# Optimization experiments

Hardware: AMD Instinct MI355X
Metric: run time of the kernel (lower is better)

Reference implementation:

```python
import jax, jax.numpy as jnp
import numpy as np

B, L, D = 512, 200, 128
N_ITEMS = 50001
T_STEPS = 4
TAU = 2.0
STEP = 1
V_TH = 1.0
SG_ALPHA = 4.0  # spikingjelly default surrogate.Sigmoid alpha


@jax.custom_vjp
def spike(x):
    return (x >= 0.0).astype(x.dtype)

def _spike_fwd(x):
    return spike(x), x

def _spike_bwd(x, g):
    s = jax.nn.sigmoid(SG_ALPHA * x)
    return (g * SG_ALPHA * s * (1.0 - s),)

spike.defvjp(_spike_fwd, _spike_bwd)


def lif_multistep(x):
    """Multi-step LIF (hard reset to 0, detach_reset). x: [T, ...] -> spikes [T, ...]."""
    def step(v, xt):
        v = v + (xt - v) / TAU  # charge (v_reset = 0)
        s = spike(v - V_TH)
        v = v - jax.lax.stop_gradient(s) * v  # hard reset, detached spike
        return v, s
    v0 = jnp.zeros_like(x[0])
    _, spikes = jax.lax.scan(step, v0, x)
    return spikes


def layernorm(x, g, b, eps=1e-5):
    m = x.mean(-1, keepdims=True)
    v = x.var(-1, keepdims=True)
    return (x - m) / jnp.sqrt(v + eps) * g + b


def _build_session_graphs(rng):
    lens = rng.integers(50, L + 1, size=B)
    item_seq = np.zeros((B, L), dtype=np.int64)
    for b in range(B):
        item_seq[b, :lens[b]] = rng.integers(1, N_ITEMS, size=lens[b])
    alias = np.zeros((B, L), dtype=np.int64)
    items = np.zeros((B, L), dtype=np.int64)
    A = np.zeros((B, L, 2 * L), dtype=np.float32)
    for b in range(B):
        u = item_seq[b]
        node = np.unique(u)  # sorted
        items[b, :len(node)] = node
        alias[b] = np.searchsorted(node, u)
        uA = np.zeros((L, L), dtype=np.float32)
        for i in range(L - 1):
            if u[i + 1] == 0:
                break
            r = np.searchsorted(node, u[i])
            c = np.searchsorted(node, u[i + 1])
            uA[r, c] = 1.0
        sin = uA.sum(0); sin[sin == 0] = 1.0
        sout = uA.sum(1); sout[sout == 0] = 1.0
        A[b, :, :L] = (uA / sin).T          # u_A_in.T
        A[b, :, L:] = ((uA.T / sout)).T     # u_A_out.T
    mask = item_seq > 0
    return A, alias, items, mask, lens.astype(np.int64)


def setup_inputs() -> dict:
    rng = np.random.default_rng(0)
    A, alias, items, mask, lens = _build_session_graphs(rng)
    stdv = 1.0 / np.sqrt(D)
    key = jax.random.key(0)
    ks = jax.random.split(key, 24)
    u = lambda k, shape: jax.random.uniform(k, shape, jnp.float32, -stdv, stdv)
    item_emb = u(ks[0], (N_ITEMS, D)).at[0].set(0.0)  # padding_idx=0
    return {
        "A": jnp.asarray(A),
        "alias_inputs": jnp.asarray(alias),
        "items": jnp.asarray(items),
        "mask": jnp.asarray(mask),
        "item_seq_len": jnp.asarray(lens),
        "item_emb": item_emb,
        "W_in": u(ks[1], (D, D)), "b_in": u(ks[2], (D,)),
        "W_out": u(ks[3], (D, D)), "b_out": u(ks[4], (D,)),
        "w_ih": u(ks[5], (3 * D, 2 * D)), "w_hh": u(ks[6], (3 * D, D)),
        "b_ih": u(ks[7], (3 * D,)), "b_hh": u(ks[8], (3 * D,)),
        "b_iah": u(ks[9], (D,)), "b_ioh": u(ks[10], (D,)),
        "W1": u(ks[11], (D, D)), "W2": u(ks[12], (D, D)),
        "W3": u(ks[13], (1, D)), "Wt": u(ks[14], (D, 2 * D)),
        "g_q": u(ks[15], (D,)), "beta_q": u(ks[16], (D,)),
        "g_sh": u(ks[17], (2 * D,)), "beta_sh": u(ks[18], (2 * D,)),
    }


def _forward(A, alias_inputs, items, mask, item_seq_len, item_emb,
             W_in, b_in, W_out, b_out, w_ih, w_hh, b_ih, b_hh, b_iah, b_ioh,
             W1, W2, W3, Wt, g_q, beta_q, g_sh, beta_sh):
    hidden = item_emb[items]  # [B,L,D]
    for _ in range(STEP):
        ein = hidden @ W_in.T + b_in
        eout = hidden @ W_out.T + b_out
        input_in = jnp.einsum('bij,bjd->bid', A[:, :, :L], ein) + b_iah
        input_out = jnp.einsum('bij,bjd->bid', A[:, :, L:], eout) + b_ioh
        inputs = jnp.concatenate([input_in, input_out], axis=-1)  # [B,L,2D]
        gi = inputs @ w_ih.T + b_ih  # [B,L,3D]
        gh = hidden @ w_hh.T + b_hh
        i_r, i_i, i_n = jnp.split(gi, 3, axis=-1)
        h_r, h_i, h_n = jnp.split(gh, 3, axis=-1)
        r = jax.nn.sigmoid(i_r + h_r)
        z = jax.nn.sigmoid(i_i + h_i)
        n = jnp.tanh(i_n + r * h_n)
        hidden = (1.0 - z) * hidden + z * n
    seq_hidden = jnp.take_along_axis(hidden, alias_inputs[..., None], axis=1)  # [B,L,D]
    ht = jnp.take_along_axis(seq_hidden, (item_seq_len - 1)[:, None, None], axis=1)[:, 0]  # [B,D]
    Qb = (ht @ W1.T)[:, None, :] + seq_hidden @ W2.T  # [B,L,D]
    Q = jnp.broadcast_to(Qb[None], (T_STEPS, B, L, D))
    Qs = lif_multistep(layernorm(Q, g_q, beta_q))
    alpha = Qs @ W3.T  # [T,B,L,1]
    mf = mask.astype(alpha.dtype)
    a = jnp.sum(alpha * seq_hidden[None] * mf[None, :, :, None], axis=2)  # [T,B,D]
    ht_T = jnp.broadcast_to(ht[None], (T_STEPS, B, D))
    sh = jnp.concatenate([a, ht_T], axis=-1)  # [T,B,2D]
    sh = layernorm(lif_multistep(sh), g_sh, beta_sh)
    return (sh @ Wt.T).mean(0)  # [B,D]


def reference(A, alias_inputs, items, mask, item_seq_len, item_emb,
              W_in, b_in, W_out, b_out, w_ih, w_hh, b_ih, b_hh, b_iah, b_ioh,
              W1, W2, W3, Wt, g_q, beta_q, g_sh, beta_sh):
    return _forward(A, alias_inputs, items, mask, item_seq_len, item_emb,
                    W_in, b_in, W_out, b_out, w_ih, w_hh, b_ih, b_hh, b_iah, b_ioh,
                    W1, W2, W3, Wt, g_q, beta_q, g_sh, beta_sh)
```

## Files before the change

### kernel.cpp

```cpp
#include <hip/hip_runtime.h>
#include <hip/hip_bf16.h>
#include <cstdint>
#include <cstddef>

#define B_ 512
#define L_ 200
#define D_ 128
#define M_ (B_*L_)
#define T_ 4

typedef short bf16x8 __attribute__((ext_vector_type(8)));
typedef unsigned short u16x8 __attribute__((ext_vector_type(8)));
typedef float f32x4 __attribute__((ext_vector_type(4)));

__device__ __forceinline__ float bf2f(unsigned short u){
  union { unsigned int i; float f; } c; c.i = ((unsigned int)u)<<16; return c.f;
}
__device__ __forceinline__ unsigned short f2bf(float f){
  union { float f; unsigned int i; } c; c.f = f;
  unsigned int r = c.i + 0x7FFFu + ((c.i>>16)&1u);
  return (unsigned short)(r>>16);
}
__device__ __forceinline__ float wsum(float v){
  #pragma unroll
  for (int m=1;m<64;m<<=1) v += __shfl_xor(v, m, 64);
  return v;
}
__device__ __forceinline__ void gload_lds16(const void* g, void* l){
  __builtin_amdgcn_global_load_lds(
      (const __attribute__((address_space(1))) void*)g,
      (__attribute__((address_space(3))) void*)l, 16, 0, 0);
}

__global__ __launch_bounds__(256)
void gemm_bt(const unsigned short* __restrict__ A, int lda,
             const unsigned short* __restrict__ Bt, int ldb,
             const float* __restrict__ bias,
             unsigned short* __restrict__ C, int ldc, int K,
             const int* __restrict__ mlimit, const int* __restrict__ gidx)
{
  const int m0 = blockIdx.y * 128;
  const int Mv = mlimit ? *mlimit : (1<<30);
  if (m0 >= Mv) return;
  __shared__ __align__(16) short sAs[2][128*32];
  __shared__ __align__(16) short sBs[2][128*32];
  const int tid = threadIdx.x;
  const int n0 = blockIdx.x * 128;
  const int lane = tid & 63;
  const int w = tid >> 6;
  const int wr = (w>>1)*64, wc = (w&1)*64;

  f32x4 acc[4][4];
  #pragma unroll
  for (int i=0;i<4;i++)
    #pragma unroll
    for (int j=0;j<4;j++) acc[i][j] = (f32x4){0.f,0.f,0.f,0.f};

  const int c1 = tid, c2 = tid + 256;
  const int r1 = c1>>2, s1 = c1&3, k1 = ((s1 ^ ((r1>>1)&3))&3)<<3;
  const int r2 = c2>>2, s2 = c2&3, k2 = ((s2 ^ ((r2>>1)&3))&3)<<3;
  int ar1 = m0 + r1, ar2 = m0 + r2;
  if (gidx){ ar1 = (ar1 < Mv) ? gidx[ar1] : 0; ar2 = (ar2 < Mv) ? gidx[ar2] : 0; }
  const int fr = lane & 15;
  const int fq = lane >> 4;
  const int fk = ((fq ^ ((fr>>1)&3))&3)<<3;

  auto stage = [&](int t){
    const int buf = t & 1, ks = t << 5;
    gload_lds16(A  + (size_t)ar1*lda + ks + k1, sAs[buf] + (size_t)c1*8);
    gload_lds16(A  + (size_t)ar2*lda + ks + k2, sAs[buf] + (size_t)c2*8);
    gload_lds16(Bt + (size_t)(n0 + r1)*ldb + ks + k1, sBs[buf] + (size_t)c1*8);
    gload_lds16(Bt + (size_t)(n0 + r2)*ldb + ks + k2, sBs[buf] + (size_t)c2*8);
  };
  const int nT = K >> 5;
  stage(0);
  __syncthreads();
  for (int t=0; t<nT; ++t){
    if (t+1 < nT) stage(t+1);
    const short* a_ = sAs[t&1];
    const short* b_ = sBs[t&1];
    bf16x8 af[4], bfr[4];
    #pragma unroll
    for (int i=0;i<4;i++){
      af[i]  = *(const bf16x8*)(a_ + (wr + i*16 + fr)*32 + fk);
      bfr[i] = *(const bf16x8*)(b_ + (wc + i*16 + fr)*32 + fk);
    }
    #pragma unroll
    for (int i=0;i<4;i++)
      #pragma unroll
      for (int j=0;j<4;j++)
        acc[i][j] = __builtin_amdgcn_mfma_f32_16x16x32_bf16(af[i], bfr[j], acc[i][j], 0,0,0);
    __syncthreads();
  }

  const int orow = fq<<2;
  #pragma unroll
  for (int i=0;i<4;i++){
    #pragma unroll
    for (int j=0;j<4;j++){
      const int gn = n0 + wc + j*16 + fr;
      const float bv = bias ? bias[gn] : 0.f;
      #pragma unroll
      for (int v=0;v<4;v++){
        const int gm = m0 + wr + i*16 + orow + v;
        C[(size_t)gm*ldc + gn] = f2bf(acc[i][j][v] + bv);
      }
    }
  }
}

__global__ __launch_bounds__(128)
void k_prepW(const float* __restrict__ w_ih, const float* __restrict__ w_hh,
             const float* __restrict__ W_in, const float* __restrict__ W_out,
             const float* __restrict__ b_in, const float* __restrict__ b_out,
             const float* __restrict__ b_ih, const float* __restrict__ b_hh,
             const float* __restrict__ b_iah, const float* __restrict__ b_ioh,
             const float* __restrict__ W2,
             const int* __restrict__ alias, const int* __restrict__ lens,
             unsigned short* __restrict__ Wbig, float* __restrict__ biasBase,
             float* __restrict__ uIn, float* __restrict__ uOut,
             unsigned short* __restrict__ w2b, int* __restrict__ nb)
{
  const int p = blockIdx.x, t = threadIdx.x;
  if (p < 128) w2b[p*128 + t] = f2bf(W2[p*128 + t]);
  const int dim = p>>2, g = p&3;
  const int row = (g==0) ? dim : (g==1) ? 128+dim : 256+dim;
  const bool has_ih = (g!=3), has_hh = (g!=2);
  __shared__ float wl[128], wrg[128], red[3][128];
  wl[t]  = has_ih ? w_ih[(size_t)row*256 + t]       : 0.f;
  wrg[t] = has_ih ? w_ih[(size_t)row*256 + 128 + t] : 0.f;
  __syncthreads();
  float cin = 0.f, cout = 0.f;
  if (has_ih) {
    for (int m=0;m<128;m++){
      cin  += wl[m]  * W_in [m*128 + t];
      cout += wrg[m] * W_out[m*128 + t];
    }
  }
  Wbig[(size_t)p*384 +       t] = f2bf(cin);
  Wbig[(size_t)p*384 + 128 + t] = f2bf(cout);
  Wbig[(size_t)p*384 + 256 + t] = f2bf(has_hh ? w_hh[(size_t)row*128 + t] : 0.f);
  red[0][t] = wl[t]*b_iah[t] + wrg[t]*b_ioh[t];
  red[1][t] = wl[t]*b_in[t];
  red[2][t] = wrg[t]*b_out[t];
  __syncthreads();
  if (t == 0) {
    float v=0.f, ui=0.f, uo=0.f;
    for (int k=0;k<128;k++){ v += red[0][k]; ui += red[1][k]; uo += red[2][k]; }
    float bb;
    if (g==0)      bb = b_ih[dim]     + b_hh[dim]     + v;
    else if (g==1) bb = b_ih[128+dim] + b_hh[128+dim] + v;
    else if (g==2) bb = b_ih[256+dim] + v;
    else           bb = b_hh[256+dim];
    biasBase[p] = bb;
    uIn[p]  = has_ih ? ui : 0.f;
    uOut[p] = has_ih ? uo : 0.f;
  }
  if (t < 64) {
    const int len = lens[p];
    int m = 0;
    for (int l=t; l<len; l+=64) m = max(m, alias[p*L_ + l]);
    #pragma unroll
    for (int o=1;o<64;o<<=1) m = max(m, __shfl_xor(m, o, 64));
    if (t==0) nb[p] = m + 1;
  }
}

__global__ __launch_bounds__(512)
void k_scan(const int* __restrict__ nb, const int* __restrict__ lens,
            int* __restrict__ nbase, int* __restrict__ vbase)
{
  __shared__ int A[2][512], Bv[2][512];
  const int t = threadIdx.x;
  const int a0 = nb[t], b0 = lens[t];
  A[0][t] = a0; Bv[0][t] = b0;
  __syncthreads();
  int cur = 0;
  for (int off=1; off<512; off<<=1){
    const int nxt = cur^1;
    A[nxt][t]  = A[cur][t]  + (t>=off ? A[cur][t-off]  : 0);
    Bv[nxt][t] = Bv[cur][t] + (t>=off ? Bv[cur][t-off] : 0);
    __syncthreads();
    cur = nxt;
  }
  nbase[t] = A[cur][t] - a0;
  vbase[t] = Bv[cur][t] - b0;
  if (t==511){ nbase[512] = A[cur][511]; vbase[512] = Bv[cur][511]; }
}

__global__ __launch_bounds__(1024)
void k_aggemb(const int* __restrict__ alias, const int* __restrict__ items,
              const int* __restrict__ lens, const float* __restrict__ emb,
              const int* __restrict__ nb, const int* __restrict__ nbase,
              const int* __restrict__ vbase,
              unsigned short* __restrict__ X3, unsigned char* __restrict__ cf,
              int* __restrict__ gidx)
{
  const int b = blockIdx.x, tid = threadIdx.x;
  __shared__ unsigned short hl[L_*128];
  __shared__ int al[L_], it[L_];
  __shared__ unsigned bmIn[L_*8], bmOut[L_*8];
  if (tid < L_) { al[tid] = alias[b*L_ + tid]; it[tid] = items[b*L_ + tid]; }
  for (int i=tid; i<L_*8; i+=1024){ bmIn[i]=0u; bmOut[i]=0u; }
  __syncthreads();
  const int len = lens[b], nB = nb[b], base = nbase[b];
  if (tid < len) gidx[vbase[b] + tid] = base + al[tid];
  if (tid < len-1) {
    const int r = al[tid], c = al[tid+1];
    atomicOr(&bmIn[c*8 + (r>>5)],  1u<<(r&31));
    atomicOr(&bmOut[r*8 + (c>>5)], 1u<<(c&31));
  }
  const int rr = tid>>5, cc = (tid&31)<<2;
  for (int s=0; s<nB; s+=32) {
    const int j = s + rr;
    if (j < nB) {
      const float4 v = *(const float4*)(emb + (size_t)it[j]*128 + cc);
      ushort4 o; o.x=f2bf(v.x); o.y=f2bf(v.y); o.z=f2bf(v.z); o.w=f2bf(v.w);
      *(ushort4*)(hl + j*128 + cc) = o;
      *(ushort4*)(X3 + (size_t)(base + j)*384 + 256 + cc) = o;
    }
  }
  __syncthreads();
  const int g = tid >> 7, d = tid & 127;
  for (int s=0; s<nB; s+=8) {
    const int i = s + g;
    if (i < nB) {
      float si=0.f, so=0.f; int ci=0, co=0;
      #pragma unroll
      for (int wd=0; wd<8; ++wd) {
        unsigned word = bmIn[i*8+wd];
        while (word) { int j = __ffs(word)-1; word &= word-1u;
          si += bf2f(hl[(wd*32+j)*128 + d]); ci++; }
        word = bmOut[i*8+wd];
        while (word) { int j = __ffs(word)-1; word &= word-1u;
          so += bf2f(hl[(wd*32+j)*128 + d]); co++; }
      }
      unsigned short* xr = X3 + (size_t)(base + i)*384;
      xr[d]       = f2bf(si / (float)(ci>0?ci:1));
      xr[128 + d] = f2bf(so / (float)(co>0?co:1));
      if (d == 0) cf[base + i] = (unsigned char)((ci>0?1:0) | (co>0?2:0));
    }
  }
}

__global__ __launch_bounds__(512)
void k_gates_gru(const unsigned short* __restrict__ X3,
                 const unsigned short* __restrict__ Wbig,
                 const float* __restrict__ biasBase,
                 const float* __restrict__ uIn,
                 const float* __restrict__ uOut,
                 const unsigned char* __restrict__ cf,
                 unsigned short* __restrict__ hidden,
                 const int* __restrict__ mlimit)
{
  const int m0 = blockIdx.y * 128;
  if (m0 >= *mlimit) return;
  __shared__ __align__(16) short sA[2][128*32];
  __shared__ __align__(16) short sB[2][256*32];
  const int tid = threadIdx.x;
  const int p0 = blockIdx.x * 256;
  const int lane = tid & 63;
  const int w = tid >> 6;
  const int wr  = (w>>2)*64;
  const int wcp = (w&3)*64;
  const int fr = lane & 15;
  const int fq = lane >> 4;
  const int fk = ((fq ^ ((fr>>1)&3))&3)<<3;

  f32x4 acc[4][4];
  #pragma unroll
  for (int i=0;i<4;i++)
    #pragma unroll
    for (int j=0;j<4;j++) acc[i][j] = (f32x4){0.f,0.f,0.f,0.f};

  const int ra = tid>>2, sa_ = tid&3, ka = ((sa_ ^ ((ra>>1)&3))&3)<<3;
  const int c1 = tid + 512, rb1 = c1>>2, sb1 = c1&3, kb1 = ((sb1 ^ ((rb1>>1)&3))&3)<<3;

  auto stage = [&](int t){
    const int buf = t & 1, ks = t << 5;
    gload_lds16(X3   + (size_t)(m0 + ra )*384 + ks + ka , sA[buf] + (size_t)tid*8);
    gload_lds16(Wbig + (size_t)(p0 + ra )*384 + ks + ka , sB[buf] + (size_t)tid*8);
    gload_lds16(Wbig + (size_t)(p0 + rb1)*384 + ks + kb1, sB[buf] + (size_t)(c1-512)*8 + 512*8);
  };
  stage(0);
  __syncthreads();
  for (int t=0; t<12; ++t){
    if (t < 11) stage(t+1);
    const short* a_ = sA[t&1];
    const short* b_ = sB[t&1];
    bf16x8 af[4], bfr[4];
    #pragma unroll
    for (int i=0;i<4;i++){
      af[i]  = *(const bf16x8*)(a_ + (wr  + i*16 + fr)*32 + fk);
      bfr[i] = *(const bf16x8*)(b_ + (wcp + i*16 + fr)*32 + fk);
    }
    #pragma unroll
    for (int i=0;i<4;i++)
      #pragma unroll
      for (int j=0;j<4;j++)
        acc[i][j] = __builtin_amdgcn_mfma_f32_16x16x32_bf16(af[i], bfr[j], acc[i][j], 0,0,0);
    __syncthreads();
  }

  const bool q0b = (lane & 1), q1b = (lane & 2);
  #pragma unroll
  for (int j=0;j<4;j++){
    const int dim = (p0>>2) + (w&3)*16 + j*4 + ((lane>>2)&3);
    const float4 bb = *(const float4*)(biasBase + dim*4);
    const float4 bi = *(const float4*)(uIn  + dim*4);
    const float4 bo = *(const float4*)(uOut + dim*4);
    #pragma unroll
    for (int i=0;i<4;i++){
      const float a0=acc[i][j][0], a1=acc[i][j][1], a2=acc[i][j][2], a3=acc[i][j][3];
      const float t0=__shfl_xor(a0,1), t1=__shfl_xor(a1,1), t2=__shfl_xor(a2,1), t3=__shfl_xor(a3,1);
      const float s0 = q0b? t1:a0, s1 = q0b? a1:t0, s2 = q0b? t3:a2, s3 = q0b? a3:t2;
      const float u0=__shfl_xor(s0,2), u1=__shfl_xor(s1,2), u2=__shfl_xor(s2,2), u3=__shfl_xor(s3,2);
      float G0 = q1b? u2:s0, G1 = q1b? u3:s1, G2 = q1b? s2:u0, G3 = q1b? s3:u1;
      const int row = m0 + wr + i*16 + fq*4 + (lane&3);
      const unsigned c = cf[row];
      const float fi = (c&1) ? 1.f : 0.f, fo = (c&2) ? 1.f : 0.f;
      G0 += bb.x + fi*bi.x + fo*bo.x;
      G1 += bb.y + fi*bi.y + fo*bo.y;
      G2 += bb.z + fi*bi.z + fo*bo.z;
      G3 += bb.w;
      const float h = bf2f(X3[(size_t)row*384 + 256 + dim]);
      const float r = 1.f/(1.f+__expf(-G0));
      const float z = 1.f/(1.f+__expf(-G1));
      const float x = G2 + r*G3;
      const float n = 1.f - 2.f/(__expf(2.f*x)+1.f);
      hidden[(size_t)row*128 + dim] = f2bf((1.f-z)*h + z*n);
    }
  }
}

__global__ __launch_bounds__(1024)
void k_attn(const unsigned short* __restrict__ Q0,
            const unsigned short* __restrict__ hidden, const int* __restrict__ gidx,
            const int* __restrict__ lens, const int* __restrict__ vbase,
            const float* __restrict__ W1,
            const float* __restrict__ g_q, const float* __restrict__ beta_q,
            const float* __restrict__ W3,
            const float* __restrict__ g_sh, const float* __restrict__ beta_sh,
            const float* __restrict__ Wt, float* __restrict__ out)
{
  const int b = blockIdx.x, tid = threadIdx.x;
  const int w = tid>>6, lane = tid&63;
  __shared__ float a_acc[16][T_][128];
  __shared__ float htv[128], htw[128];
  __shared__ float ys[256];
  __shared__ float part[T_][4];
  const int len = lens[b], vb = vbase[b];
  for (int i=tid; i<16*T_*128; i+=1024) ((float*)a_acc)[i] = 0.f;
  if (tid < 128) htv[tid] = bf2f(hidden[(size_t)gidx[vb + len - 1]*128 + tid]);
  __syncthreads();
  {
    const int d = tid >> 3, seg = (tid & 7) << 4;
    const float* wr1 = W1 + (size_t)d*128 + seg;
    const float* hv = htv + seg;
    float p = 0.f;
    #pragma unroll
    for (int k=0;k<16;k++) p += wr1[k]*hv[k];
    p += __shfl_xor(p, 1, 64); p += __shfl_xor(p, 2, 64); p += __shfl_xor(p, 4, 64);
    if ((tid & 7) == 0) htw[d] = p;
  }
  __syncthreads();
  const float h0 = htw[lane], h1 = htw[lane+64];
  const float gq0 = g_q[lane], gq1 = g_q[lane+64];
  const float bq0 = beta_q[lane], bq1 = beta_q[lane+64];
  const float w30 = W3[lane], w31 = W3[lane+64];
  for (int l = w; l < len; l += 16) {
    const size_t row = (size_t)(vb + l);
    const size_t hrow = (size_t)gidx[row];
    const float q0 = bf2f(Q0[row*128 + lane]) + h0;
    const float q1 = bf2f(Q0[row*128 + lane + 64]) + h1;
    float s1 = q0 + q1, s2 = q0*q0 + q1*q1;
    #pragma unroll
    for (int mm=1;mm<64;mm<<=1){
      s1 += __shfl_xor(s1, mm, 64);
      s2 += __shfl_xor(s2, mm, 64);
    }
    const float m = s1 * (1.f/128.f);
    const float var = fmaxf(s2 * (1.f/128.f) - m*m, 0.f);
    const float inv = rsqrtf(var + 1e-5f);
    const float x0 = (q0-m)*inv*gq0 + bq0;
    const float x1 = (q1-m)*inv*gq1 + bq1;
    const float sh0 = bf2f(hidden[hrow*128+lane]), sh1 = bf2f(hidden[hrow*128+lane+64]);
    float pa[T_];
    float v0=0.f, v1=0.f;
    #pragma unroll
    for (int t=0;t<T_;t++){
      v0 = 0.5f*(v0+x0); v1 = 0.5f*(v1+x1);
      const float s0 = (v0>=1.f)?1.f:0.f, s1v = (v1>=1.f)?1.f:0.f;
      v0 -= s0*v0; v1 -= s1v*v1;
      pa[t] = s0*w30 + s1v*w31;
    }
    #pragma unroll
    for (int mm=1;mm<64;mm<<=1){
      pa[0] += __shfl_xor(pa[0], mm, 64);
      pa[1] += __shfl_xor(pa[1], mm, 64);
      pa[2] += __shfl_xor(pa[2], mm, 64);
      pa[3] += __shfl_xor(pa[3], mm, 64);
    }
    #pragma unroll
    for (int t=0;t<T_;t++){
      a_acc[w][t][lane]    += pa[t]*sh0;
      a_acc[w][t][lane+64] += pa[t]*sh1;
    }
  }
  __syncthreads();

  float sp[T_] = {0.f,0.f,0.f,0.f};
  if (tid < 256) {
    const float xh = (tid >= 128) ? htv[tid-128] : 0.f;
    float v = 0.f;
    #pragma unroll
    for (int t=0;t<T_;t++){
      float x;
      if (tid < 128) {
        x = 0.f;
        #pragma unroll
        for (int p=0;p<16;p++) x += a_acc[p][t][tid];
      } else x = xh;
      v = 0.5f*(v + x);
      const float s = (v>=1.f)?1.f:0.f;
      v -= s*v;
      sp[t] = s;
    }
    #pragma unroll
    for (int t=0;t<T_;t++){
      const float r = wsum(sp[t]);
      if (lane==0) part[t][w] = r;
    }
  }
  __syncthreads();
  if (tid < 256) {
    float acc4 = 0.f;
    #pragma unroll
    for (int t=0;t<T_;t++){
      const float k = part[t][0]+part[t][1]+part[t][2]+part[t][3];
      const float mean = k * (1.f/256.f);
      const float varr = mean - mean*mean;
      const float inv = rsqrtf(varr + 1e-5f);
      acc4 += (sp[t]-mean)*inv;
    }
    ys[tid] = acc4*g_sh[tid] + 4.f*beta_sh[tid];
  }
  __syncthreads();
  if (tid < 128) {
    float acc = 0.f;
    const float4* wr4 = (const float4*)(Wt + (size_t)tid*256);
    const float4* ys4 = (const float4*)ys;
    #pragma unroll 8
    for (int k=0;k<64;k++){
      const float4 wv = wr4[k], yv = ys4[k];
      acc += wv.x*yv.x + wv.y*yv.y + wv.z*yv.z + wv.w*yv.w;
    }
    out[(size_t)b*128 + tid] = acc*0.25f;
  }
}

extern "C" void kernel_launch(void* const* d_in, const int* in_sizes, int n_in,
                              void* d_out, int out_size, void* d_ws, size_t ws_size,
                              hipStream_t stream)
{
  const int*   alias  = (const int*)d_in[1];
  const int*   items  = (const int*)d_in[2];
  const int*   lens   = (const int*)d_in[4];
  const float* emb    = (const float*)d_in[5];
  const float* W_in   = (const float*)d_in[6];
  const float* b_in   = (const float*)d_in[7];
  const float* W_out  = (const float*)d_in[8];
  const float* b_out  = (const float*)d_in[9];
  const float* w_ih   = (const float*)d_in[10];
  const float* w_hh   = (const float*)d_in[11];
  const float* b_ih   = (const float*)d_in[12];
  const float* b_hh   = (const float*)d_in[13];
  const float* b_iah  = (const float*)d_in[14];
  const float* b_ioh  = (const float*)d_in[15];
  const float* W1     = (const float*)d_in[16];
  const float* W2     = (const float*)d_in[17];
  const float* W3     = (const float*)d_in[18];
  const float* Wt     = (const float*)d_in[19];
  const float* g_q    = (const float*)d_in[20];
  const float* beta_q = (const float*)d_in[21];
  const float* g_sh   = (const float*)d_in[22];
  const float* beta_sh= (const float*)d_in[23];

  char* ws = (char*)d_ws;
  size_t off = 0;
  auto alloc = [&](size_t bytes)->void* {
    void* p = ws + off; off += (bytes + 255) & ~(size_t)255; return p;
  };
  unsigned short* X3    = (unsigned short*)alloc((size_t)M_*384*2);
  unsigned short* hidden= (unsigned short*)alloc((size_t)M_*128*2);
  unsigned short* Q0c   = (unsigned short*)alloc((size_t)M_*128*2);
  int*            gidx  = (int*)alloc((size_t)M_*4);
  unsigned short* Wbig  = (unsigned short*)alloc((size_t)512*384*2);
  unsigned short* w2b   = (unsigned short*)alloc(16384*2);
  float*          biasBase = (float*)alloc(512*4);
  float*          uIn   = (float*)alloc(512*4);
  float*          uOut  = (float*)alloc(512*4);
  unsigned char*  cf    = (unsigned char*)alloc(M_);
  int*            nb    = (int*)alloc(512*4);
  int*            nbase = (int*)alloc(513*4);
  int*            vbase = (int*)alloc(513*4);
  if (off > ws_size) return;

  k_prepW<<<512,128,0,stream>>>(w_ih,w_hh,W_in,W_out,b_in,b_out,b_ih,b_hh,
                                b_iah,b_ioh,W2,alias,lens,
                                Wbig,biasBase,uIn,uOut,w2b,nb);
  k_scan<<<1,512,0,stream>>>(nb, lens, nbase, vbase);
  k_aggemb<<<B_,1024,0,stream>>>(alias, items, lens, emb, nb, nbase, vbase,
                                 X3, cf, gidx);
  k_gates_gru<<<dim3(2,800),512,0,stream>>>(X3, Wbig, biasBase, uIn, uOut, cf,
                                            hidden, nbase+512);
  gemm_bt<<<dim3(1,800),256,0,stream>>>(hidden, 128, w2b, 128, nullptr, Q0c, 128,
                                        128, vbase+512, gidx);
  k_attn<<<B_,1024,0,stream>>>(Q0c, hidden, gidx, lens, vbase, W1, g_q, beta_q,
                               W3, g_sh, beta_sh, Wt, (float*)d_out);
}
```

Before: 177.4 us.

## Fold prefix scan into aggemb and stage GRU hidden tile through LDS

Removes the separate single-block scan kernel: every aggemb block now recomputes the 512-entry prefix sums of node counts and lengths in shared memory, and block b writes its own offsets. This saves one launch and its serialization, but repeats a 9-step scan with barriers in all 512 blocks. Separately, the GRU epilogue now loads the previous-hidden tile from X3 into LDS with a swizzled async load, replacing scattered 2-byte global reads, at the cost of an extra barrier.

```diff
diff --git a/kernel.cpp b/kernel.cpp
--- a/kernel.cpp
+++ b/kernel.cpp
@@ -166,45 +166,39 @@
   }
 }
 
-__global__ __launch_bounds__(512)
-void k_scan(const int* __restrict__ nb, const int* __restrict__ lens,
-            int* __restrict__ nbase, int* __restrict__ vbase)
-{
-  __shared__ int A[2][512], Bv[2][512];
-  const int t = threadIdx.x;
-  const int a0 = nb[t], b0 = lens[t];
-  A[0][t] = a0; Bv[0][t] = b0;
-  __syncthreads();
-  int cur = 0;
-  for (int off=1; off<512; off<<=1){
-    const int nxt = cur^1;
-    A[nxt][t]  = A[cur][t]  + (t>=off ? A[cur][t-off]  : 0);
-    Bv[nxt][t] = Bv[cur][t] + (t>=off ? Bv[cur][t-off] : 0);
-    __syncthreads();
-    cur = nxt;
-  }
-  nbase[t] = A[cur][t] - a0;
-  vbase[t] = Bv[cur][t] - b0;
-  if (t==511){ nbase[512] = A[cur][511]; vbase[512] = Bv[cur][511]; }
-}
-
 __global__ __launch_bounds__(1024)
 void k_aggemb(const int* __restrict__ alias, const int* __restrict__ items,
               const int* __restrict__ lens, const float* __restrict__ emb,
-              const int* __restrict__ nb, const int* __restrict__ nbase,
-              const int* __restrict__ vbase,
+              const int* __restrict__ nb,
               unsigned short* __restrict__ X3, unsigned char* __restrict__ cf,
-              int* __restrict__ gidx)
+              int* __restrict__ gidx, int* __restrict__ nbase,
+              int* __restrict__ vbase)
 {
   const int b = blockIdx.x, tid = threadIdx.x;
   __shared__ unsigned short hl[L_*128];
   __shared__ int al[L_], it[L_];
   __shared__ unsigned bmIn[L_*8], bmOut[L_*8];
+  __shared__ int scN[2][512], scV[2][512];
   if (tid < L_) { al[tid] = alias[b*L_ + tid]; it[tid] = items[b*L_ + tid]; }
   for (int i=tid; i<L_*8; i+=1024){ bmIn[i]=0u; bmOut[i]=0u; }
-  __syncthreads();
-  const int len = lens[b], nB = nb[b], base = nbase[b];
-  if (tid < len) gidx[vbase[b] + tid] = base + al[tid];
+  if (tid < 512){ scN[0][tid] = nb[tid]; scV[0][tid] = lens[tid]; }
+  __syncthreads();
+  int cur = 0;
+  for (int off=1; off<512; off<<=1){
+    const int nxt = cur^1;
+    if (tid < 512){
+      scN[nxt][tid] = scN[cur][tid] + (tid>=off ? scN[cur][tid-off] : 0);
+      scV[nxt][tid] = scV[cur][tid] + (tid>=off ? scV[cur][tid-off] : 0);
+    }
+    __syncthreads();
+    cur = nxt;
+  }
+  const int len = lens[b], nB = nb[b];
+  const int base = scN[cur][b] - nB;
+  const int vb   = scV[cur][b] - len;
+  if (tid == 0){ nbase[b] = base; vbase[b] = vb; }
+  if (tid == 1){ nbase[512] = scN[cur][511]; vbase[512] = scV[cur][511]; }
+  if (tid < len) gidx[vb + tid] = base + al[tid];
   if (tid < len-1) {
     const int r = al[tid], c = al[tid+1];
     atomicOr(&bmIn[c*8 + (r>>5)],  1u<<(r&31));
@@ -302,10 +296,23 @@
     __syncthreads();
   }
 
+  short* sH = &sB[0][0];
+  const int dbase = p0 >> 2;
+  #pragma unroll
+  for (int q=0;q<2;q++){
+    const int c = tid + q*512;
+    const int rowl = c >> 3, ccp = c & 7;
+    const int ccs = ccp ^ (rowl & 7);
+    gload_lds16(X3 + (size_t)(m0 + rowl)*384 + 256 + dbase + ccs*8,
+                sH + (size_t)c*8);
+  }
+  __syncthreads();
+
   const bool q0b = (lane & 1), q1b = (lane & 2);
   #pragma unroll
   for (int j=0;j<4;j++){
-    const int dim = (p0>>2) + (w&3)*16 + j*4 + ((lane>>2)&3);
+    const int dim = dbase + (w&3)*16 + j*4 + ((lane>>2)&3);
+    const int dl = dim - dbase;
     const float4 bb = *(const float4*)(biasBase + dim*4);
     const float4 bi = *(const float4*)(uIn  + dim*4);
     const float4 bo = *(const float4*)(uOut + dim*4);
@@ -317,13 +324,15 @@
       const float u0=__shfl_xor(s0,2), u1=__shfl_xor(s1,2), u2=__shfl_xor(s2,2), u3=__shfl_xor(s3,2);
       float G0 = q1b? u2:s0, G1 = q1b? u3:s1, G2 = q1b? s2:u0, G3 = q1b? s3:u1;
       const int row = m0 + wr + i*16 + fq*4 + (lane&3);
+      const int rl = row - m0;
       const unsigned c = cf[row];
       const float fi = (c&1) ? 1.f : 0.f, fo = (c&2) ? 1.f : 0.f;
       G0 += bb.x + fi*bi.x + fo*bo.x;
       G1 += bb.y + fi*bi.y + fo*bo.y;
       G2 += bb.z + fi*bi.z + fo*bo.z;
       G3 += bb.w;
-      const float h = bf2f(X3[(size_t)row*384 + 256 + dim]);
+      const float h = bf2f((unsigned short)
+          sH[rl*64 + (((dl>>3) ^ (rl&7))<<3) + (dl&7)]);
       const float r = 1.f/(1.f+__expf(-G0));
       const float z = 1.f/(1.f+__expf(-G1));
       const float x = G2 + r*G3;
@@ -509,9 +518,8 @@
   k_prepW<<<512,128,0,stream>>>(w_ih,w_hh,W_in,W_out,b_in,b_out,b_ih,b_hh,
                                 b_iah,b_ioh,W2,alias,lens,
                                 Wbig,biasBase,uIn,uOut,w2b,nb);
-  k_scan<<<1,512,0,stream>>>(nb, lens, nbase, vbase);
-  k_aggemb<<<B_,1024,0,stream>>>(alias, items, lens, emb, nb, nbase, vbase,
-                                 X3, cf, gidx);
+  k_aggemb<<<B_,1024,0,stream>>>(alias, items, lens, emb, nb,
+                                 X3, cf, gidx, nbase, vbase);
   k_gates_gru<<<dim3(2,800),512,0,stream>>>(X3, Wbig, biasBase, uIn, uOut, cf,
                                             hidden, nbase+512);
   gemm_bt<<<dim3(1,800),256,0,stream>>>(hidden, 128, w2b, 128, nullptr, Q0c, 128,
```

Result: no change. 175.1 us (-1.3%).
